# Performance work log

Measured on AMD Instinct MI355X. Metric: run time of the kernel, lower is better.

Reference implementation:

```python
import jax, jax.numpy as jnp
import numpy as np

NF = 64      # feature channels
DG = 8       # deformable groups
B, H, W = 4, 128, 128
K = 3        # kernel size
TAPS = K * K # 9 sampling taps per pixel per group


def _conv(x, w, b):
    # 3x3 stride-1 SAME conv, NCHW / OIHW
    y = jax.lax.conv_general_dilated(x, w, (1, 1), 'SAME',
                                     dimension_numbers=('NCHW', 'OIHW', 'NCHW'))
    return y + b[None, :, None, None]


def _lrelu(x):
    return jnp.where(x >= 0, x, 0.1 * x)


def _deform_conv(x, off_y, off_x, mask, w, b):
    """Modulated deformable conv v2 (3x3, stride 1, pad 1, dilation 1).
    x:     [B, C, H, W]
    off_y/off_x/mask: [B, dg, 9, H, W]
    w:     [Cout, C, 3, 3], b: [Cout]
    """
    Bn, C, Hn, Wn = x.shape
    dg = off_y.shape[1]
    cg = C // dg
    k = jnp.arange(K, dtype=x.dtype) - (K - 1) / 2  # [-1, 0, 1]
    ky = jnp.repeat(k, K)  # [9] row offsets
    kx = jnp.tile(k, K)    # [9] col offsets
    base_y = jnp.arange(Hn, dtype=x.dtype)[:, None]   # [H,1]
    base_x = jnp.arange(Wn, dtype=x.dtype)[None, :]   # [1,W]
    sy = off_y + ky[None, None, :, None, None] + base_y  # [B,dg,9,H,W]
    sx = off_x + kx[None, None, :, None, None] + base_x
    y0 = jnp.floor(sy)
    x0 = jnp.floor(sx)
    xg = x.reshape(Bn, dg, cg, Hn * Wn)
    val = jnp.zeros((Bn, dg, cg, TAPS, Hn, Wn), x.dtype)
    # bilinear interpolation over 4 corners, zero outside image
    for di in (0.0, 1.0):
        for dj in (0.0, 1.0):
            yi = y0 + di
            xi = x0 + dj
            wgt = (1.0 - jnp.abs(sy - yi)) * (1.0 - jnp.abs(sx - xi))
            valid = (yi >= 0) & (yi < Hn) & (xi >= 0) & (xi < Wn)
            idx = (jnp.clip(yi, 0, Hn - 1).astype(jnp.int32) * Wn
                   + jnp.clip(xi, 0, Wn - 1).astype(jnp.int32))  # [B,dg,9,H,W]
            g = jnp.take_along_axis(
                xg, idx.reshape(Bn, dg, 1, TAPS * Hn * Wn), axis=-1
            ).reshape(Bn, dg, cg, TAPS, Hn, Wn)
            val = val + (wgt * valid.astype(x.dtype))[:, :, None] * g
    val = val * mask[:, :, None]  # modulation
    out = jnp.einsum('bgckhw,ogck->bohw', val,
                     w.reshape(w.shape[0], dg, cg, TAPS))
    return out + b[None, :, None, None]


def setup_inputs() -> dict:
    key = jax.random.key(0)
    ks = jax.random.split(key, 12)
    s = lambda fan: 1.0 / np.sqrt(fan)
    return {
        'nbr': jax.random.normal(ks[0], (B, NF, H, W), jnp.float32),
        'ref': jax.random.normal(ks[1], (B, NF, H, W), jnp.float32),
        'w_off1': jax.random.normal(ks[2], (NF, 2 * NF, K, K), jnp.float32) * s(2 * NF * 9),
        'b_off1': jnp.zeros((NF,), jnp.float32),
        'w_off2': jax.random.normal(ks[3], (NF, NF, K, K), jnp.float32) * s(NF * 9),
        'b_off2': jnp.zeros((NF,), jnp.float32),
        # offset/mask conv: small init keeps sampled offsets modest (as trained DCNs do)
        'w_om': jax.random.normal(ks[4], (3 * DG * TAPS, NF, K, K), jnp.float32) * 0.01,
        'b_om': jnp.zeros((3 * DG * TAPS,), jnp.float32),
        'w_dcn': jax.random.normal(ks[5], (NF, NF, K, K), jnp.float32) * s(NF * 9),
        'b_dcn': jnp.zeros((NF,), jnp.float32),
    }


def reference(nbr, ref, w_off1, b_off1, w_off2, b_off2, w_om, b_om, w_dcn, b_dcn):
    off = _lrelu(_conv(jnp.concatenate([nbr, ref], axis=1), w_off1, b_off1))
    off = _lrelu(_conv(off, w_off2, b_off2))
    om = _conv(off, w_om, b_om)                 # [B, 3*dg*9, H, W]
    o1, o2, m = jnp.split(om, 3, axis=1)        # each [B, dg*9, H, W]
    Bn, _, Hn, Wn = nbr.shape
    off_y = o1.reshape(Bn, DG, TAPS, Hn, Wn)
    off_x = o2.reshape(Bn, DG, TAPS, Hn, Wn)
    mask = jax.nn.sigmoid(m).reshape(Bn, DG, TAPS, Hn, Wn)
    fea = _deform_conv(nbr, off_y, off_x, mask, w_dcn, b_dcn)
    return fea
```

## Files before the change

### kernel.cpp

```cpp
#include <hip/hip_runtime.h>
#include <hip/hip_bf16.h>
#include <math.h>

#define H_DIM 128
#define W_DIM 128
#define BATCH 4
#define HW (H_DIM * W_DIM)

typedef __attribute__((ext_vector_type(8))) short bf16x8;
typedef __attribute__((ext_vector_type(4))) short s16x4;
typedef __attribute__((ext_vector_type(4))) float f32x4;
typedef __attribute__((ext_vector_type(4))) unsigned int u32x4;
typedef _Float16 f16x2 __attribute__((ext_vector_type(2)));
typedef _Float16 f16x8 __attribute__((ext_vector_type(8)));

static __device__ __forceinline__ unsigned short f2bf(float f) {
    __hip_bfloat16 h = __float2bfloat16(f);
    return *reinterpret_cast<unsigned short*>(&h);
}
static __device__ __forceinline__ float bf2f(unsigned short u) {
    return __uint_as_float(((unsigned int)u) << 16);
}
static __device__ __forceinline__ unsigned short f2h(float f) {
    _Float16 h = (_Float16)f;
    return *reinterpret_cast<unsigned short*>(&h);
}

__global__ __launch_bounds__(256)
void prep_nhwc_kernel(const float* __restrict__ nbr, const float* __restrict__ ref,
                      unsigned short* __restrict__ dst,
                      unsigned short* __restrict__ gmaj) {
    __shared__ float s[128][65];
    const int b  = blockIdx.y;
    const int p0 = blockIdx.x * 64;
    const int t  = threadIdx.x;
    const int px = t & 63;
#pragma unroll
    for (int it = 0; it < 32; ++it) {
        int c = it * 4 + (t >> 6);
        const float* src = (c < 64) ? nbr : ref;
        int cs = c & 63;
        s[c][px] = src[(size_t)(b * 64 + cs) * HW + p0 + px];
    }
    __syncthreads();
#pragma unroll
    for (int it = 0; it < 4; ++it) {
        int idx = it * 256 + t;
        int p  = idx >> 4;
        int ut = idx & 15;
        int x  = (p0 + p) & 127;
        int key = (x + 1) & 7;
        int cpos = (ut & 8) | ((ut & 7) ^ key);
        bf16x8 v;
#pragma unroll
        for (int j = 0; j < 8; ++j)
            v[j] = (short)f2bf(s[ut * 8 + j][p]);
        *(bf16x8*)(dst + ((size_t)(b * HW + p0 + p) * 128 + cpos * 8)) = v;
    }
#pragma unroll
    for (int it = 0; it < 2; ++it) {
        int idx = it * 256 + t;
        int g   = idx >> 6;
        int p2  = idx & 63;
        bf16x8 v;
#pragma unroll
        for (int j = 0; j < 8; ++j)
            v[j] = (short)f2h(s[g * 8 + j][p2]);
        *(bf16x8*)(gmaj + ((size_t)(b * 8 + g) * HW + p0 + p2) * 8) = v;
    }
}

__global__ void pack_all_kernel(const float* __restrict__ w1, const float* __restrict__ w2,
                                const float* __restrict__ wom, const float* __restrict__ wdcn,
                                unsigned short* __restrict__ wpk1, unsigned short* __restrict__ wpk2,
                                unsigned short* __restrict__ wpk3, unsigned short* __restrict__ wpkD) {
    int idx = blockIdx.x * 256 + threadIdx.x;
    const int N1 = 73728, N2 = 36864, N3 = 129024, N4 = 36864;
    const float* w; unsigned short* dst; int CIN, NCF, COUT; bool asF16 = false;
    if (idx < N1)                { w = w1;   dst = wpk1; CIN = 128; NCF = 4;  COUT = 64; }
    else if (idx < N1+N2)        { idx -= N1;       w = w2;   dst = wpk2; CIN = 64; NCF = 4;  COUT = 64; }
    else if (idx < N1+N2+N3)     { idx -= N1+N2;    w = wom;  dst = wpk3; CIN = 64; NCF = 14; COUT = 216; }
    else if (idx < N1+N2+N3+N4)  { idx -= N1+N2+N3; w = wdcn; dst = wpkD; CIN = 64; NCF = 4;  COUT = 64; asF16 = true; }
    else return;
    int j    = idx & 7;
    int lane = (idx >> 3) & 63;
    int frag = idx >> 9;
    int cf   = frag % NCF;
    int ks   = frag / NCF;
    int co = cf * 16 + (lane & 15);
    int k  = ks * 32 + (lane >> 4) * 8 + j;
    int t  = k / CIN;
    int ci = k % CIN;
    float v = (co < COUT) ? w[((size_t)co * CIN + ci) * 9 + t] : 0.f;
    dst[idx] = asF16 ? f2h(v) : f2bf(v);
}

template<int CIN, int NKS, bool RELU>
__global__ __launch_bounds__(256, 3)
void conv64_mfma_kernel(const unsigned short* __restrict__ in,
                        const unsigned short* __restrict__ wpk,
                        const float* __restrict__ bias,
                        unsigned short* __restrict__ out)
{
    constexpr int ROWB = 66 * CIN * 2;
    __shared__ __align__(16) char smem[3 * ROWB];

    const int rb   = blockIdx.x;
    const int x0   = (rb & 1) * 64;
    const int y    = (rb >> 1) & 127;
    const int b    = rb >> 8;
    const int tid  = threadIdx.x;
    const int lane = tid & 63;
    const int wave = tid >> 6;
    const int l15  = lane & 15;
    const int q    = lane >> 4;
    const u32x4 zv = {0u, 0u, 0u, 0u};

    const int lstart = (x0 == 0) ? 1 : 0;
    const int lzero  = (x0 == 0) ? 0 : 65;
    for (int dy = 0; dy < 3; ++dy) {
        int yy = y + dy - 1;
        char* dstrow = smem + dy * ROWB;
        if (yy >= 0 && yy < H_DIM) {
            const char* src = (const char*)(in +
                ((size_t)(b * H_DIM + yy) * W_DIM + (x0 - 1 + lstart)) * CIN);
            for (int i = tid * 16; i < 65 * CIN * 2; i += 256 * 16)
                *(u32x4*)(dstrow + lstart * CIN * 2 + i) = *(const u32x4*)(src + i);
            if (tid < CIN / 8)
                *(u32x4*)(dstrow + lzero * CIN * 2 + tid * 16) = zv;
        } else {
            for (int i = tid * 16; i < 66 * CIN * 2; i += 256 * 16)
                *(u32x4*)(dstrow + i) = zv;
        }
    }
    __syncthreads();

    f32x4 acc[4];
#pragma unroll
    for (int pf = 0; pf < 4; ++pf)
        acc[pf] = (f32x4){0.f, 0.f, 0.f, 0.f};

#pragma unroll
    for (int ks = 0; ks < NKS; ++ks) {
        const int t   = ks / (CIN / 32);
        const int ci0 = (ks % (CIN / 32)) * 32;
        const int dy = t / 3, dx = t % 3;
        const int u  = (ci0 >> 3) + q;
        bf16x8 a[4];
#pragma unroll
        for (int pf = 0; pf < 4; ++pf) {
            const int l = pf * 16 + l15 + dx;
            const int upos = u ^ (l & 7);
            a[pf] = *(const bf16x8*)(smem + dy * ROWB + (l * CIN + upos * 8) * 2);
        }
        bf16x8 wfr = *(const bf16x8*)(wpk + ((size_t)(ks * 4 + wave) * 64 + lane) * 8);
#pragma unroll
        for (int pf = 0; pf < 4; ++pf)
            acc[pf] = __builtin_amdgcn_mfma_f32_16x16x32_bf16(a[pf], wfr, acc[pf], 0, 0, 0);
    }

    const int co = wave * 16 + l15;
    const float bv = bias[co];
#pragma unroll
    for (int pf = 0; pf < 4; ++pf)
#pragma unroll
        for (int r = 0; r < 4; ++r) {
            int x = x0 + pf * 16 + q * 4 + r;
            float v = acc[pf][r] + bv;
            if (RELU) v = (v >= 0.f) ? v : 0.1f * v;
            int cpos = (((co >> 3) ^ ((x + 1) & 7)) << 3) | (co & 7);
            out[((size_t)(b * H_DIM + y) * W_DIM + x) * 64 + cpos] = f2bf(v);
        }
}

struct GSlot {
    f16x8 c00, c01, c10, c11;
    f16x2 w00, w01, w10, w11;
};

__global__ __launch_bounds__(256, 4)
void fused_om_deform_kernel(const unsigned short* __restrict__ in,
                            const unsigned short* __restrict__ xg,
                            const unsigned short* __restrict__ wpk3,
                            const unsigned short* __restrict__ wpkD,
                            const float* __restrict__ bom,
                            const float* __restrict__ bdcn,
                            float* __restrict__ out)
{
    constexpr int ROWB = 34 * 64 * 2;
    constexpr int OMST = 48;
    __shared__ __align__(16) char smem[216 * OMST * 2 + 2 * 64 * 20 * 4];
    unsigned short* om_lds = (unsigned short*)smem;
    float* red = (float*)(smem + 216 * OMST * 2);

    const int hwid = blockIdx.x;
    const int rb   = (hwid & 7) * (BATCH * H_DIM * 4 / 8) + (hwid >> 3);
    const int x0   = (rb & 3) * 32;
    const int y    = (rb >> 2) & 127;
    const int b    = rb >> 9;
    const int tid  = threadIdx.x;
    const int lane = tid & 63;
    const int wave = tid >> 6;
    const int l15  = lane & 15;
    const int q    = lane >> 4;
    const u32x4 zv = {0u, 0u, 0u, 0u};

    {
        const int c0 = (x0 == 0) ? 1 : 0;
        const int c1 = (x0 == 96) ? 33 : 34;
        const int nbytes = (c1 - c0) * 128;
        for (int dy = 0; dy < 3; ++dy) {
            int yy = y + dy - 1;
            char* dstrow = smem + dy * ROWB;
            if (yy >= 0 && yy < H_DIM) {
                const char* src = (const char*)(in +
                    ((size_t)(b * H_DIM + yy) * W_DIM + (x0 - 1 + c0)) * 64);
                for (int i = tid * 16; i < nbytes; i += 256 * 16)
                    *(u32x4*)(dstrow + c0 * 128 + i) = *(const u32x4*)(src + i);
                if (x0 == 0 && tid < 8)
                    *(u32x4*)(dstrow + 0 * 128 + tid * 16) = zv;
                if (x0 == 96 && tid < 8)
                    *(u32x4*)(dstrow + 33 * 128 + tid * 16) = zv;
            } else {
                for (int i = tid * 16; i < 34 * 128; i += 256 * 16)
                    *(u32x4*)(dstrow + i) = zv;
            }
        }
    }
    __syncthreads();

    {
        f32x4 acc[2][4];
#pragma unroll
        for (int pf = 0; pf < 2; ++pf)
#pragma unroll
            for (int cfi = 0; cfi < 4; ++cfi)
                acc[pf][cfi] = (f32x4){0.f, 0.f, 0.f, 0.f};

#pragma unroll
        for (int ks = 0; ks < 18; ++ks) {
            const int t   = ks >> 1;
            const int ci0 = (ks & 1) * 32;
            const int dy = t / 3, dx = t % 3;
            bf16x8 a[2];
#pragma unroll
            for (int pf = 0; pf < 2; ++pf) {
                const int l = pf * 16 + l15 + dx;
                const int upos = ((ci0 >> 3) + q) ^ (l & 7);
                a[pf] = *(const bf16x8*)(smem + dy * ROWB + (l * 64 + upos * 8) * 2);
            }
#pragma unroll
            for (int cfi = 0; cfi < 4; ++cfi) {
                const int cf = wave + cfi * 4;
                if (cfi < 3 || wave < 2) {
                    bf16x8 wfr = *(const bf16x8*)(wpk3 + ((size_t)(ks * 14 + cf) * 64 + lane) * 8);
                    acc[0][cfi] = __builtin_amdgcn_mfma_f32_16x16x32_bf16(a[0], wfr, acc[0][cfi], 0, 0, 0);
                    acc[1][cfi] = __builtin_amdgcn_mfma_f32_16x16x32_bf16(a[1], wfr, acc[1][cfi], 0, 0, 0);
                }
            }
        }
        __syncthreads();

#pragma unroll
        for (int cfi = 0; cfi < 4; ++cfi) {
            const int cf = wave + cfi * 4;
            if (cfi < 3 || wave < 2) {
                const int co = cf * 16 + l15;
                if (co < 216) {
                    const float bv = bom[co];
#pragma unroll
                    for (int pf = 0; pf < 2; ++pf) {
                        s16x4 pk;
#pragma unroll
                        for (int r = 0; r < 4; ++r)
                            pk[r] = (short)f2bf(acc[pf][cfi][r] + bv);
                        *(s16x4*)(om_lds + co * OMST + pf * 16 + q * 4) = pk;
                    }
                }
            }
        }
    }
    __syncthreads();

    const int pxgrp = wave >> 1;
    const int khalf = wave & 1;
    const int kbase = khalf * 9;
    const int px0w  = pxgrp * 16;
    const int xl    = px0w + l15;
    const int x     = x0 + xl;

    f32x4 acc2[4];
#pragma unroll
    for (int cf = 0; cf < 4; ++cf)
        acc2[cf] = (f32x4){0.f, 0.f, 0.f, 0.f};

    auto OMLOAD = [&](int i, float& oy, float& ox, float& mr) {
        const int ks  = kbase + i;
        const int och = ((ks & 1) * 4 + q) * 9 + (ks >> 1);
        oy = bf2f(om_lds[och * OMST + xl]);
        ox = bf2f(om_lds[(72 + och) * OMST + xl]);
        mr = bf2f(om_lds[(144 + och) * OMST + xl]);
    };

    auto GPREP = [&](int i, float oy, float ox, float mr, GSlot& s) {
        const int ks  = kbase + i;
        const int tap = ks >> 1;
        const int g   = (ks & 1) * 4 + q;
        const int dy  = tap / 3 - 1;
        const int dx  = tap % 3 - 1;
        const float mask = 1.f / (1.f + __expf(-mr));

        const float sy = oy + (float)(dy + y);
        const float sx = ox + (float)(dx + x);
        const float fy = floorf(sy);
        const float fx = floorf(sx);
        const int y0  = (int)fy;
        const int xq0 = (int)fx;
        const float ay = sy - fy;
        const float ax = sx - fx;

        const bool vy0 = (y0 >= 0) && (y0 < H_DIM);
        const bool vy1 = (y0 >= -1) && (y0 < H_DIM - 1);
        const bool vx0 = (xq0 >= 0) && (xq0 < W_DIM);
        const bool vx1 = (xq0 >= -1) && (xq0 < W_DIM - 1);

        float w00 = (1.f - ay) * (1.f - ax); if (!(vy0 && vx0)) w00 = 0.f;
        float w01 = (1.f - ay) * ax;         if (!(vy0 && vx1)) w01 = 0.f;
        float w10 = ay * (1.f - ax);         if (!(vy1 && vx0)) w10 = 0.f;
        float w11 = ay * ax;                 if (!(vy1 && vx1)) w11 = 0.f;
        w00 *= mask; w01 *= mask; w10 *= mask; w11 *= mask;
        { _Float16 h = (_Float16)w00; s.w00 = (f16x2){h, h}; }
        { _Float16 h = (_Float16)w01; s.w01 = (f16x2){h, h}; }
        { _Float16 h = (_Float16)w10; s.w10 = (f16x2){h, h}; }
        { _Float16 h = (_Float16)w11; s.w11 = (f16x2){h, h}; }

        const int iy0 = min(max(y0, 0), H_DIM - 1);
        const int iy1 = min(max(y0 + 1, 0), H_DIM - 1);
        const int ix0 = min(max(xq0, 0), W_DIM - 1);
        const int ix1 = min(max(xq0 + 1, 0), W_DIM - 1);

        const unsigned short* gb = xg + (size_t)(b * 8 + g) * HW * 8;
        s.c00 = *(const f16x8*)(gb + (size_t)(iy0 * W_DIM + ix0) * 8);
        s.c01 = *(const f16x8*)(gb + (size_t)(iy0 * W_DIM + ix1) * 8);
        s.c10 = *(const f16x8*)(gb + (size_t)(iy1 * W_DIM + ix0) * 8);
        s.c11 = *(const f16x8*)(gb + (size_t)(iy1 * W_DIM + ix1) * 8);
    };

    auto CONSUME = [&](int i, GSlot& s) {
        const int ks = kbase + i;
        f16x8 av;
        const f16x2* c00 = reinterpret_cast<const f16x2*>(&s.c00);
        const f16x2* c01 = reinterpret_cast<const f16x2*>(&s.c01);
        const f16x2* c10 = reinterpret_cast<const f16x2*>(&s.c10);
        const f16x2* c11 = reinterpret_cast<const f16x2*>(&s.c11);
        f16x2* avp = reinterpret_cast<f16x2*>(&av);
#pragma unroll
        for (int j = 0; j < 4; ++j)
            avp[j] = s.w00 * c00[j] + s.w01 * c01[j]
                   + s.w10 * c10[j] + s.w11 * c11[j];
#pragma unroll
        for (int cf = 0; cf < 4; ++cf) {
            f16x8 wfr = *(const f16x8*)(wpkD + ((size_t)(ks * 4 + cf) * 64 + lane) * 8);
            acc2[cf] = __builtin_amdgcn_mfma_f32_16x16x32_f16(av, wfr, acc2[cf], 0, 0, 0);
        }
    };

    {
        float oyA, oxA, mrA, oyB, oxB, mrB;
        GSlot GA, GB;
        OMLOAD(0, oyA, oxA, mrA);
        OMLOAD(1, oyB, oxB, mrB);
        GPREP(0, oyA, oxA, mrA, GA);
#pragma unroll
        for (int i = 0; i < 8; i += 2) {
            OMLOAD(i + 2, oyA, oxA, mrA);
            GPREP(i + 1, oyB, oxB, mrB, GB);
            CONSUME(i, GA);
            if (i + 3 < 9) OMLOAD(i + 3, oyB, oxB, mrB);
            GPREP(i + 2, oyA, oxA, mrA, GA);
            CONSUME(i + 1, GB);
        }
        CONSUME(8, GA);
    }

    if (khalf == 1) {
#pragma unroll
        for (int cf = 0; cf < 4; ++cf)
            *(f32x4*)&red[((size_t)pxgrp * 64 + lane) * 20 + cf * 4] = acc2[cf];
    }
    __syncthreads();
    if (khalf == 0) {
#pragma unroll
        for (int cf = 0; cf < 4; ++cf) {
            const f32x4 other = *(const f32x4*)&red[((size_t)pxgrp * 64 + lane) * 20 + cf * 4];
            const int co = cf * 16 + l15;
            const float bv = bdcn[co];
#pragma unroll
            for (int r = 0; r < 4; ++r) {
                int xs = x0 + px0w + q * 4 + r;
                __builtin_nontemporal_store(acc2[cf][r] + other[r] + bv,
                    out + (size_t)(b * 64 + co) * HW + y * W_DIM + xs);
            }
        }
    }
}

extern "C" void kernel_launch(void* const* d_in, const int* in_sizes, int n_in,
                              void* d_out, int out_size, void* d_ws, size_t ws_size,
                              hipStream_t stream) {
    const float* nbr  = (const float*)d_in[0];
    const float* ref  = (const float*)d_in[1];
    const float* w1   = (const float*)d_in[2];
    const float* b1   = (const float*)d_in[3];
    const float* w2   = (const float*)d_in[4];
    const float* b2   = (const float*)d_in[5];
    const float* wom  = (const float*)d_in[6];
    const float* bom  = (const float*)d_in[7];
    const float* wdcn = (const float*)d_in[8];
    const float* bdcn = (const float*)d_in[9];
    float* out = (float*)d_out;
    char* W = (char*)d_ws;

    unsigned short* in1  = (unsigned short*)(W + 0);
    unsigned short* c1o  = (unsigned short*)(W + 16777216);
    unsigned short* c2o  = (unsigned short*)(W + 25165824);
    unsigned short* nbrg = (unsigned short*)(W + 33554432);
    unsigned short* wpk1 = (unsigned short*)(W + 41943040);
    unsigned short* wpk2 = (unsigned short*)(W + 42090496);
    unsigned short* wpk3 = (unsigned short*)(W + 42164224);
    unsigned short* wpkD = (unsigned short*)(W + 42422272);

    prep_nhwc_kernel<<<dim3(HW / 64, BATCH), 256, 0, stream>>>(nbr, ref, in1, nbrg);
    pack_all_kernel<<<1080, 256, 0, stream>>>(w1, w2, wom, wdcn,
                                              wpk1, wpk2, wpk3, wpkD);

    conv64_mfma_kernel<128, 36, true>
        <<<dim3(BATCH * H_DIM * 2), 256, 0, stream>>>(in1, wpk1, b1, c1o);
    conv64_mfma_kernel<64, 18, true>
        <<<dim3(BATCH * H_DIM * 2), 256, 0, stream>>>(c1o, wpk2, b2, c2o);

    fused_om_deform_kernel<<<dim3(BATCH * H_DIM * 4), 256, 0, stream>>>(
        c2o, nbrg, wpk3, wpkD, bom, bdcn, out);
}
```

Measured before the change: 99.17 us.

## Software-pipeline deform gathers and weight loads with inline asm and explicit vmcnt waits

After: 101.0 us. Within noise of the previous version (+1.8%).

```diff
diff --git a/kernel.cpp b/kernel.cpp
--- a/kernel.cpp
+++ b/kernel.cpp
@@ -173,12 +173,21 @@
         }
 }
 
-struct GSlot {
+struct PSlot {
     f16x8 c00, c01, c10, c11;
-    f16x2 w00, w01, w10, w11;
+    f16x8 w0, w1, w2, w3;
+    f16x2 h00, h01, h10, h11;
 };
 
-__global__ __launch_bounds__(256, 4)
+#define GLOAD(dst, addr) \
+    asm volatile("global_load_dwordx4 %0, %1, off" : "=v"(dst) : "v"(addr))
+#define GLOADO(dst, addr, OFF) \
+    asm volatile("global_load_dwordx4 %0, %1, off offset:" #OFF : "=v"(dst) : "v"(addr))
+#define VMWAIT(N) do { \
+    asm volatile("s_waitcnt vmcnt(" #N ")" ::: "memory"); \
+    __builtin_amdgcn_sched_barrier(0); } while (0)
+
+__global__ __launch_bounds__(256, 3)
 void fused_om_deform_kernel(const unsigned short* __restrict__ in,
                             const unsigned short* __restrict__ xg,
                             const unsigned short* __restrict__ wpk3,
@@ -294,16 +303,13 @@
     for (int cf = 0; cf < 4; ++cf)
         acc2[cf] = (f32x4){0.f, 0.f, 0.f, 0.f};
 
-    auto OMLOAD = [&](int i, float& oy, float& ox, float& mr) {
+    auto PREP = [&](int i, PSlot& s) {
         const int ks  = kbase + i;
         const int och = ((ks & 1) * 4 + q) * 9 + (ks >> 1);
-        oy = bf2f(om_lds[och * OMST + xl]);
-        ox = bf2f(om_lds[(72 + och) * OMST + xl]);
-        mr = bf2f(om_lds[(144 + och) * OMST + xl]);
-    };
-
-    auto GPREP = [&](int i, float oy, float ox, float mr, GSlot& s) {
-        const int ks  = kbase + i;
+        const float oy = bf2f(om_lds[och * OMST + xl]);
+        const float ox = bf2f(om_lds[(72 + och) * OMST + xl]);
+        const float mr = bf2f(om_lds[(144 + och) * OMST + xl]);
+
         const int tap = ks >> 1;
         const int g   = (ks & 1) * 4 + q;
         const int dy  = tap / 3 - 1;
@@ -329,25 +335,33 @@
         float w10 = ay * (1.f - ax);         if (!(vy1 && vx0)) w10 = 0.f;
         float w11 = ay * ax;                 if (!(vy1 && vx1)) w11 = 0.f;
         w00 *= mask; w01 *= mask; w10 *= mask; w11 *= mask;
-        { _Float16 h = (_Float16)w00; s.w00 = (f16x2){h, h}; }
-        { _Float16 h = (_Float16)w01; s.w01 = (f16x2){h, h}; }
-        { _Float16 h = (_Float16)w10; s.w10 = (f16x2){h, h}; }
-        { _Float16 h = (_Float16)w11; s.w11 = (f16x2){h, h}; }
+        { _Float16 h = (_Float16)w00; s.h00 = (f16x2){h, h}; }
+        { _Float16 h = (_Float16)w01; s.h01 = (f16x2){h, h}; }
+        { _Float16 h = (_Float16)w10; s.h10 = (f16x2){h, h}; }
+        { _Float16 h = (_Float16)w11; s.h11 = (f16x2){h, h}; }
 
         const int iy0 = min(max(y0, 0), H_DIM - 1);
         const int iy1 = min(max(y0 + 1, 0), H_DIM - 1);
         const int ix0 = min(max(xq0, 0), W_DIM - 1);
         const int ix1 = min(max(xq0 + 1, 0), W_DIM - 1);
 
-        const unsigned short* gb = xg + (size_t)(b * 8 + g) * HW * 8;
-        s.c00 = *(const f16x8*)(gb + (size_t)(iy0 * W_DIM + ix0) * 8);
-        s.c01 = *(const f16x8*)(gb + (size_t)(iy0 * W_DIM + ix1) * 8);
-        s.c10 = *(const f16x8*)(gb + (size_t)(iy1 * W_DIM + ix0) * 8);
-        s.c11 = *(const f16x8*)(gb + (size_t)(iy1 * W_DIM + ix1) * 8);
+        const unsigned short* gb  = xg + (size_t)(b * 8 + g) * HW * 8;
+        const unsigned short* a00 = gb + (size_t)(iy0 * W_DIM + ix0) * 8;
+        const unsigned short* a01 = gb + (size_t)(iy0 * W_DIM + ix1) * 8;
+        const unsigned short* a10 = gb + (size_t)(iy1 * W_DIM + ix0) * 8;
+        const unsigned short* a11 = gb + (size_t)(iy1 * W_DIM + ix1) * 8;
+        GLOAD(s.c00, a00);
+        GLOAD(s.c01, a01);
+        GLOAD(s.c10, a10);
+        GLOAD(s.c11, a11);
+        const unsigned short* wp = wpkD + ((size_t)(ks * 4) * 64 + lane) * 8;
+        GLOAD (s.w0, wp);
+        GLOADO(s.w1, wp, 1024);
+        GLOADO(s.w2, wp, 2048);
+        GLOADO(s.w3, wp, 3072);
     };
 
-    auto CONSUME = [&](int i, GSlot& s) {
-        const int ks = kbase + i;
+    auto CONSUME = [&](PSlot& s) {
         f16x8 av;
         const f16x2* c00 = reinterpret_cast<const f16x2*>(&s.c00);
         const f16x2* c01 = reinterpret_cast<const f16x2*>(&s.c01);
@@ -356,31 +370,27 @@
         f16x2* avp = reinterpret_cast<f16x2*>(&av);
 #pragma unroll
         for (int j = 0; j < 4; ++j)
-            avp[j] = s.w00 * c00[j] + s.w01 * c01[j]
-                   + s.w10 * c10[j] + s.w11 * c11[j];
-#pragma unroll
-        for (int cf = 0; cf < 4; ++cf) {
-            f16x8 wfr = *(const f16x8*)(wpkD + ((size_t)(ks * 4 + cf) * 64 + lane) * 8);
-            acc2[cf] = __builtin_amdgcn_mfma_f32_16x16x32_f16(av, wfr, acc2[cf], 0, 0, 0);
-        }
+            avp[j] = s.h00 * c00[j] + s.h01 * c01[j]
+                   + s.h10 * c10[j] + s.h11 * c11[j];
+        acc2[0] = __builtin_amdgcn_mfma_f32_16x16x32_f16(av, s.w0, acc2[0], 0, 0, 0);
+        acc2[1] = __builtin_amdgcn_mfma_f32_16x16x32_f16(av, s.w1, acc2[1], 0, 0, 0);
+        acc2[2] = __builtin_amdgcn_mfma_f32_16x16x32_f16(av, s.w2, acc2[2], 0, 0, 0);
+        acc2[3] = __builtin_amdgcn_mfma_f32_16x16x32_f16(av, s.w3, acc2[3], 0, 0, 0);
     };
 
     {
-        float oyA, oxA, mrA, oyB, oxB, mrB;
-        GSlot GA, GB;
-        OMLOAD(0, oyA, oxA, mrA);
-        OMLOAD(1, oyB, oxB, mrB);
-        GPREP(0, oyA, oxA, mrA, GA);
-#pragma unroll
-        for (int i = 0; i < 8; i += 2) {
-            OMLOAD(i + 2, oyA, oxA, mrA);
-            GPREP(i + 1, oyB, oxB, mrB, GB);
-            CONSUME(i, GA);
-            if (i + 3 < 9) OMLOAD(i + 3, oyB, oxB, mrB);
-            GPREP(i + 2, oyA, oxA, mrA, GA);
-            CONSUME(i + 1, GB);
-        }
-        CONSUME(8, GA);
+        PSlot SA, SB;
+        PREP(0, SA);
+        PREP(1, SB);
+        VMWAIT(8); CONSUME(SA); PREP(2, SA);
+        VMWAIT(8); CONSUME(SB); PREP(3, SB);
+        VMWAIT(8); CONSUME(SA); PREP(4, SA);
+        VMWAIT(8); CONSUME(SB); PREP(5, SB);
+        VMWAIT(8); CONSUME(SA); PREP(6, SA);
+        VMWAIT(8); CONSUME(SB); PREP(7, SB);
+        VMWAIT(8); CONSUME(SA); PREP(8, SA);
+        VMWAIT(8); CONSUME(SB);
+        VMWAIT(0); CONSUME(SA);
     }
 
     if (khalf == 1) {
```
